# Kernel tuning notes

Measured on AMD Instinct MI355X. Metric: run time of the kernel, lower is better.

## Reference

```python
import jax, jax.numpy as jnp
import numpy as np

M, N, IN_DIM, NITER = 32, 32, 1024, 100
ALPHA, SIGMA = 0.3, 16.0  # sigma default = max(m, n) / 2
BATCH = 16384


def setup_inputs() -> dict:
    key = jax.random.key(0)
    k1, k2 = jax.random.split(key)
    x = jax.random.normal(k1, (BATCH, IN_DIM), dtype=jnp.float32)
    weights = jax.random.normal(k2, (IN_DIM, M * N), dtype=jnp.float32)
    ii, jj = jnp.meshgrid(jnp.arange(M), jnp.arange(N), indexing='ij')
    locations = jnp.stack([ii.ravel(), jj.ravel()], axis=1).astype(jnp.int32)  # (m*n, 2), row-major like the generator
    return {"x": x, "weights": weights, "locations": locations, "current_iter": 10}


def reference(x, weights, locations, current_iter):
    # x: (B, in_dim); weights: (in_dim, m*n); locations: (m*n, 2)
    B = x.shape[0]
    # Euclidean distances from each sample to each neuron, via ||a-b||^2 expansion
    x2 = jnp.sum(x * x, axis=1, keepdims=True)            # (B, 1)
    w2 = jnp.sum(weights * weights, axis=0)[None, :]      # (1, m*n)
    d2 = jnp.clip(x2 + w2 - 2.0 * (x @ weights), 0.0, None)
    dists = jnp.sqrt(d2)                                  # (B, m*n)
    loss_per = jnp.min(dists, axis=1)                     # (B,)
    bmu_index = jnp.argmin(dists, axis=1)                 # (B,)
    iter_correction = 1.0 - current_iter / NITER
    lr = ALPHA * iter_correction
    sigma = SIGMA * iter_correction
    loc_f = locations.astype(jnp.float32)                 # (m*n, 2)
    bmu_loc = loc_f[bmu_index]                            # (B, 2)
    # squared grid distance of every neuron to each sample's BMU
    dsq = jnp.sum((loc_f[None, :, :] - bmu_loc[:, None, :]) ** 2, axis=2)  # (B, m*n)
    lr_locations = jnp.exp(-dsq / (sigma * sigma)) * lr   # (B, m*n)
    # delta[i,k] = (1/B) * sum_b lr_locations[b,k] * (x[b,i] - weights[i,k])
    # computed without materializing the (B, in_dim, m*n) broadcast tensor
    pos = jnp.einsum('bk,bi->ik', lr_locations, x)        # (in_dim, m*n)
    neg = weights * jnp.sum(lr_locations, axis=0)[None, :]
    delta = (pos - neg) / B
    new_weights = weights + delta
    loss = jnp.sum(loss_per) / B
    return loss, new_weights
```

## Files before the change

kernel.cpp:

```cpp
#include <hip/hip_runtime.h>

typedef unsigned short u16;
typedef short bf16x8 __attribute__((ext_vector_type(8)));
typedef float f32x4 __attribute__((ext_vector_type(4)));

#define BATCH   16384
#define INDIM   1024
#define KNEUR   1024

__device__ __forceinline__ u16 f2bf(float f) {
  union { float f; unsigned u; } v; v.f = f;
  unsigned r = v.u + 0x7FFFu + ((v.u >> 16) & 1u);
  return (u16)(r >> 16);
}
__device__ __forceinline__ float bf2f(u16 h) {
  union { unsigned u; float f; } v; v.u = ((unsigned)h) << 16; return v.f;
}

#define GLDS(gp, lp) __builtin_amdgcn_global_load_lds( \
  (const __attribute__((address_space(1))) void*)(gp), \
  (__attribute__((address_space(3))) void*)(lp), 16, 0, 0)

__global__ __launch_bounds__(256)
void k_prep(const float* __restrict__ x, u16* __restrict__ xb, float* __restrict__ x2,
            const float* __restrict__ w, u16* __restrict__ wt, float* __restrict__ w2,
            const int* __restrict__ loc, const int* __restrict__ itp,
            u16* __restrict__ Tb, float* __restrict__ Tf,
            float* __restrict__ Xf, int* __restrict__ cntcur, float* __restrict__ S) {
  __shared__ float tile[64][65];
  __shared__ float red[4][64];
  int bid = blockIdx.x;
  int t = threadIdx.x;
  if (bid < 4096) {
    int row = bid * 4 + (t >> 6);
    int l = t & 63;
    const float* xr = x + (size_t)row * INDIM;
    u16* xbr = xb + (size_t)row * INDIM;
    float s = 0.f;
    #pragma unroll
    for (int seg = 0; seg < 4; ++seg) {
      float4 v = *(const float4*)(xr + seg * 256 + l * 4);
      ushort4 o; o.x = f2bf(v.x); o.y = f2bf(v.y); o.z = f2bf(v.z); o.w = f2bf(v.w);
      *(ushort4*)(xbr + seg * 256 + l * 4) = o;
      s += v.x * v.x + v.y * v.y + v.z * v.z + v.w * v.w;
    }
    for (int m = 32; m; m >>= 1) s += __shfl_xor(s, m, 64);
    if (l == 0) x2[row] = s;
  } else if (bid < 8192) {
    int id = (bid - 4096) * 256 + t;
    int c = id >> 10, k = id & 1023;
    float corr = 1.f - (float)itp[0] / 100.f;
    float lr = 0.3f * corr;
    float sig = 16.f * corr;
    float inv_s2 = 1.f / (sig * sig);
    int di = loc[2 * c] - loc[2 * k];
    int dj = loc[2 * c + 1] - loc[2 * k + 1];
    float v = lr * __expf(-(float)(di * di + dj * dj) * inv_s2);
    Tf[id] = v;
    Tb[id] = f2bf(v);
    Xf[id] = 0.f;
    if (id < 2048) cntcur[id] = 0;
    if (id < 1024) S[id] = 0.f;
  } else if (bid < 8448) {
    int bb = bid - 8192;
    int bi = bb & 15;
    int bj = bb >> 4;
    int tx = t & 63, ty = t >> 6;
    int i0 = bj * 64, k0 = bi * 64;
    for (int r = ty; r < 64; r += 4)
      tile[r][tx] = w[(size_t)(i0 + r) * KNEUR + k0 + tx];
    __syncthreads();
    for (int r = ty; r < 64; r += 4)
      wt[(size_t)(k0 + r) * INDIM + i0 + tx] = f2bf(tile[tx][r]);
  } else {
    int tx = t & 63, ty = t >> 6;
    int k = (bid - 8448) * 64 + tx;
    float s = 0.f;
    for (int i = ty * 256; i < ty * 256 + 256; ++i) {
      float v = w[(size_t)i * KNEUR + k];
      s += v * v;
    }
    red[ty][tx] = s;
    __syncthreads();
    if (ty == 0) w2[k] = red[0][tx] + red[1][tx] + red[2][tx] + red[3][tx];
  }
}

template <int EPI>
__global__ __launch_bounds__(256, 4)
void k_gemm(const u16* __restrict__ A, const u16* __restrict__ Bm,
            const float* __restrict__ x2, const float* __restrict__ w2,
            float* __restrict__ pmin, int* __restrict__ pidx,
            float* __restrict__ P4) {
  __shared__ __align__(16) u16 ldsA[128 * 64];
  __shared__ __align__(16) u16 ldsB[128 * 64];
  __shared__ float s_rv[2][128];
  __shared__ int   s_ri[2][128];

  int bid = blockIdx.x;
  int mb, nb, ktlo, kthi, ks;
  if (EPI == 1) {
    int swz = (bid & 7) * 128 + (bid >> 3);
    mb = swz >> 3; nb = swz & 7;
    ktlo = 0; kthi = 16; ks = 0;
  } else {
    ks = bid & 3;
    int tile = bid >> 2;
    mb = tile >> 3; nb = tile & 7;
    ktlo = ks * 4; kthi = ktlo + 4;
  }
  int lane = threadIdx.x & 63;
  int wid = threadIdx.x >> 6;
  int wr = wid >> 1, wc = wid & 1;

  f32x4 acc[4][4];
  #pragma unroll
  for (int i = 0; i < 4; ++i)
    #pragma unroll
    for (int j = 0; j < 4; ++j) { acc[i][j][0] = 0.f; acc[i][j][1] = 0.f; acc[i][j][2] = 0.f; acc[i][j][3] = 0.f; }

  const size_t rowA0 = (size_t)mb * 128;
  const size_t rowB0 = (size_t)nb * 128;

  for (int kt = ktlo; kt < kthi; ++kt) {
    int k0 = kt * 64;
    __syncthreads();
    #pragma unroll
    for (int q = 0; q < 4; ++q) {
      int p = q * 256 + wid * 64 + lane;
      int row = p >> 3;
      int clog = (p & 7) ^ (row & 7);
      GLDS(A + (rowA0 + row) * 1024 + k0 + clog * 8,
           ldsA + (size_t)(q * 256 + wid * 64) * 8);
    }
    #pragma unroll
    for (int q = 0; q < 4; ++q) {
      int p = q * 256 + wid * 64 + lane;
      int row = p >> 3;
      int clog = (p & 7) ^ (row & 7);
      GLDS(Bm + (rowB0 + row) * 1024 + k0 + clog * 8,
           ldsB + (size_t)(q * 256 + wid * 64) * 8);
    }
    __syncthreads();
    #pragma unroll
    for (int kk = 0; kk < 2; ++kk) {
      bf16x8 af[4], bfr[4];
      #pragma unroll
      for (int mt = 0; mt < 4; ++mt) {
        int row = wr * 64 + mt * 16 + (lane & 15);
        int ch = (kk * 4 + (lane >> 4)) ^ (row & 7);
        af[mt] = *(const bf16x8*)(ldsA + row * 64 + ch * 8);
      }
      #pragma unroll
      for (int nt = 0; nt < 4; ++nt) {
        int row = wc * 64 + nt * 16 + (lane & 15);
        int ch = (kk * 4 + (lane >> 4)) ^ (row & 7);
        bfr[nt] = *(const bf16x8*)(ldsB + row * 64 + ch * 8);
      }
      #pragma unroll
      for (int mt = 0; mt < 4; ++mt)
        #pragma unroll
        for (int nt = 0; nt < 4; ++nt)
          acc[mt][nt] = __builtin_amdgcn_mfma_f32_16x16x32_bf16(af[mt], bfr[nt], acc[mt][nt], 0, 0, 0);
    }
  }

  if (EPI == 1) {
    int g = lane >> 4;
    int li = lane & 15;
    #pragma unroll
    for (int mt = 0; mt < 4; ++mt) {
      #pragma unroll
      for (int r = 0; r < 4; ++r) {
        int rowl = wr * 64 + mt * 16 + g * 4 + r;
        float xv = x2[rowA0 + rowl];
        float v = 1e30f; int vi = 0;
        #pragma unroll
        for (int nt = 0; nt < 4; ++nt) {
          int col = (int)rowB0 + wc * 64 + nt * 16 + li;
          float d2 = xv + w2[col] - 2.f * acc[mt][nt][r];
          if (d2 < v) { v = d2; vi = col; }
        }
        #pragma unroll
        for (int m = 1; m < 16; m <<= 1) {
          float ov = __shfl_xor(v, m, 64);
          int oi = __shfl_xor(vi, m, 64);
          if (ov < v || (ov == v && oi < vi)) { v = ov; vi = oi; }
        }
        if (li == 0) { s_rv[wc][rowl] = v; s_ri[wc][rowl] = vi; }
      }
    }
    __syncthreads();
    int t = threadIdx.x;
    if (t < 128) {
      float v0 = s_rv[0][t], v1 = s_rv[1][t];
      int i0 = s_ri[0][t], i1 = s_ri[1][t];
      float v = v0; int vi = i0;
      if (v1 < v0) { v = v1; vi = i1; }
      size_t brow = rowA0 + t;
      pmin[brow * 8 + nb] = v;
      pidx[brow * 8 + nb] = vi;
    }
  } else {
    float* base = P4 + ((size_t)ks << 20);
    #pragma unroll
    for (int mt = 0; mt < 4; ++mt)
      #pragma unroll
      for (int nt = 0; nt < 4; ++nt)
        #pragma unroll
        for (int r = 0; r < 4; ++r) {
          int i = (int)rowA0 + wr * 64 + mt * 16 + (lane >> 4) * 4 + r;
          int k = (int)rowB0 + wc * 64 + nt * 16 + (lane & 15);
          base[(size_t)i * KNEUR + k] = acc[mt][nt][r];
        }
  }
}

__global__ void k_bmu_count(const float* __restrict__ pmin, const int* __restrict__ pidx,
                            int* __restrict__ bmu, float* __restrict__ lpart,
                            int* __restrict__ cnt) {
  int b = blockIdx.x * 256 + threadIdx.x;
  float v = 1e30f; int vi = 0;
  #pragma unroll
  for (int j = 0; j < 8; ++j) {
    float pv = pmin[(size_t)b * 8 + j];
    if (pv < v) { v = pv; vi = pidx[(size_t)b * 8 + j]; }
  }
  bmu[b] = vi;
  atomicAdd(&cnt[vi], 1);
  float d = sqrtf(fmaxf(v, 0.f));
  __shared__ float red[256];
  red[threadIdx.x] = d;
  __syncthreads();
  for (int s = 128; s > 0; s >>= 1) {
    if (threadIdx.x < s) red[threadIdx.x] += red[threadIdx.x + s];
    __syncthreads();
  }
  if (threadIdx.x == 0) lpart[blockIdx.x] = red[0];
}

__global__ void k_offsets_loss(const int* __restrict__ cnt, int* __restrict__ cursor,
                               float* __restrict__ cntf,
                               const float* __restrict__ lpart, float* __restrict__ out) {
  __shared__ int sc[256];
  int t = threadIdx.x;
  int4 c4 = *(const int4*)(cnt + 4 * t);
  int tsum = c4.x + c4.y + c4.z + c4.w;
  sc[t] = tsum;
  __syncthreads();
  for (int off = 1; off < 256; off <<= 1) {
    int val = sc[t];
    int add = (t >= off) ? sc[t - off] : 0;
    __syncthreads();
    sc[t] = val + add;
    __syncthreads();
  }
  int excl = sc[t] - tsum;
  cursor[4 * t + 0] = excl;
  cursor[4 * t + 1] = excl + c4.x;
  cursor[4 * t + 2] = excl + c4.x + c4.y;
  cursor[4 * t + 3] = excl + c4.x + c4.y + c4.z;
  cntf[4 * t + 0] = (float)c4.x;
  cntf[4 * t + 1] = (float)c4.y;
  cntf[4 * t + 2] = (float)c4.z;
  cntf[4 * t + 3] = (float)c4.w;
  if (t < 64) {
    float l = lpart[t];
    for (int m = 32; m; m >>= 1) l += __shfl_xor(l, m, 64);
    if (t == 0) out[0] = l * (1.f / (float)BATCH);
  }
}

__global__ void k_place_S(const int* __restrict__ bmu, int* __restrict__ cursor,
                          int* __restrict__ perm,
                          const float* __restrict__ cntf, const float* __restrict__ Tf,
                          float* __restrict__ S) {
  int bid = blockIdx.x;
  int t = threadIdx.x;
  if (bid < 64) {
    int b = bid * 256 + t;
    int c = bmu[b];
    int p = atomicAdd(&cursor[c], 1);
    perm[p] = b;
  } else {
    int chunk = bid - 64;
    int cchunk = chunk >> 2;
    int kb = chunk & 3;
    int k = kb * 256 + t;
    float s = 0.f;
    for (int c = cchunk * 64; c < cchunk * 64 + 64; ++c)
      s += cntf[c] * Tf[(size_t)c * KNEUR + k];
    atomicAdd(&S[k], s);
  }
}

__global__ __launch_bounds__(256)
void k_xsum2(const int* __restrict__ perm, const int* __restrict__ bmu,
             const u16* __restrict__ xb, float* __restrict__ Xf) {
  int t = threadIdx.x;
  int m0 = blockIdx.x * 16;
  int pm[16], cl[16];
  #pragma unroll
  for (int j = 0; j < 16; ++j) pm[j] = perm[m0 + j];
  #pragma unroll
  for (int j = 0; j < 16; ++j) cl[j] = bmu[pm[j]];
  float a0 = 0.f, a1 = 0.f, a2 = 0.f, a3 = 0.f;
  int ccur = cl[0];
  #pragma unroll
  for (int j = 0; j < 16; ++j) {
    if (cl[j] != ccur) {
      float* p = Xf + (size_t)ccur * INDIM + 4 * t;
      atomicAdd(p + 0, a0); atomicAdd(p + 1, a1);
      atomicAdd(p + 2, a2); atomicAdd(p + 3, a3);
      a0 = a1 = a2 = a3 = 0.f;
      ccur = cl[j];
    }
    ushort4 v = *(const ushort4*)(xb + (size_t)pm[j] * INDIM + t * 4);
    a0 += bf2f(v.x); a1 += bf2f(v.y); a2 += bf2f(v.z); a3 += bf2f(v.w);
  }
  float* p = Xf + (size_t)ccur * INDIM + 4 * t;
  atomicAdd(p + 0, a0); atomicAdd(p + 1, a1);
  atomicAdd(p + 2, a2); atomicAdd(p + 3, a3);
}

__global__ void k_trans_base(const float* __restrict__ Xf, u16* __restrict__ xst,
                             const float* __restrict__ w, const float* __restrict__ S,
                             float* __restrict__ outw) {
  int bid = blockIdx.x;
  int t = threadIdx.x;
  if (bid < 256) {
    __shared__ float tile[64][65];
    int bc = bid & 15;
    int bi = bid >> 4;
    int tx = t & 63, ty = t >> 6;
    int c0 = bc * 64, i0 = bi * 64;
    for (int r = ty; r < 64; r += 4)
      tile[r][tx] = Xf[(size_t)(c0 + r) * INDIM + i0 + tx];
    __syncthreads();
    for (int r = ty; r < 64; r += 4)
      xst[(size_t)(i0 + r) * KNEUR + c0 + tx] = f2bf(tile[tx][r]);
  } else {
    const float invB = 1.f / (float)BATCH;
    size_t base = ((size_t)(bid - 256) * 256 + t) * 16;
    int k = (int)(base & 1023);
    #pragma unroll
    for (int seg = 0; seg < 4; ++seg) {
      float4 wv = *(const float4*)(w + base + seg * 4);
      float4 sv = *(const float4*)(S + k + seg * 4);
      outw[base + seg * 4 + 0] = wv.x - wv.x * sv.x * invB;
      outw[base + seg * 4 + 1] = wv.y - wv.y * sv.y * invB;
      outw[base + seg * 4 + 2] = wv.z - wv.z * sv.z * invB;
      outw[base + seg * 4 + 3] = wv.w - wv.w * sv.w * invB;
    }
  }
}

__global__ void k_wupd(const float* __restrict__ P4, float* __restrict__ outw) {
  const float invB = 1.f / (float)BATCH;
  int id4 = blockIdx.x * 256 + threadIdx.x;
  size_t base = (size_t)id4 * 4;
  float4 p0 = *(const float4*)(P4 + base);
  float4 p1 = *(const float4*)(P4 + (1u << 20) + base);
  float4 p2 = *(const float4*)(P4 + (2u << 20) + base);
  float4 p3 = *(const float4*)(P4 + (3u << 20) + base);
  outw[base + 0] += (p0.x + p1.x + p2.x + p3.x) * invB;
  outw[base + 1] += (p0.y + p1.y + p2.y + p3.y) * invB;
  outw[base + 2] += (p0.z + p1.z + p2.z + p3.z) * invB;
  outw[base + 3] += (p0.w + p1.w + p2.w + p3.w) * invB;
}

extern "C" void kernel_launch(void* const* d_in, const int* in_sizes, int n_in,
                              void* d_out, int out_size, void* d_ws, size_t ws_size,
                              hipStream_t stream) {
  const float* x = (const float*)d_in[0];
  const float* w = (const float*)d_in[1];
  const int* loc = (const int*)d_in[2];
  const int* it = (const int*)d_in[3];
  float* out = (float*)d_out;

  char* ws = (char*)d_ws;
  size_t off = 0;
  auto alloc = [&](size_t bytes) -> void* {
    void* p = ws + off;
    off += (bytes + 255) & ~(size_t)255;
    return p;
  };
  u16* xb    = (u16*)  alloc((size_t)BATCH * INDIM * 2);
  u16* wt    = (u16*)  alloc((size_t)KNEUR * INDIM * 2);
  u16* Tb    = (u16*)  alloc((size_t)KNEUR * KNEUR * 2);
  float* Tf  = (float*)alloc((size_t)KNEUR * KNEUR * 4);
  u16* xst   = (u16*)  alloc((size_t)INDIM * KNEUR * 2);
  float* x2  = (float*)alloc((size_t)BATCH * 4);
  float* w2  = (float*)alloc((size_t)KNEUR * 4);
  float* pmin= (float*)alloc((size_t)BATCH * 8 * 4);
  int* pidx  = (int*)  alloc((size_t)BATCH * 8 * 4);
  int* bmu   = (int*)  alloc((size_t)BATCH * 4);
  float* cntf= (float*)alloc((size_t)KNEUR * 4);
  float* S   = (float*)alloc((size_t)KNEUR * 4);
  float* lpart=(float*)alloc(64 * 4);
  float* Xf  = (float*)alloc((size_t)KNEUR * INDIM * 4);
  int* cntcur= (int*)  alloc((size_t)2 * KNEUR * 4);
  int* perm  = (int*)  alloc((size_t)BATCH * 4);
  if (off > ws_size) return;

  int* cnt = cntcur;
  int* cursor = cntcur + KNEUR;
  float* outw = out + 1;
  float* P4 = (float*)xb;

  k_prep<<<8464, 256, 0, stream>>>(x, xb, x2, w, wt, w2, loc, it, Tb, Tf, Xf, cntcur, S);
  k_gemm<1><<<1024, 256, 0, stream>>>(xb, wt, x2, w2, pmin, pidx, nullptr);
  k_bmu_count<<<64, 256, 0, stream>>>(pmin, pidx, bmu, lpart, cnt);
  k_offsets_loss<<<1, 256, 0, stream>>>(cnt, cursor, cntf, lpart, out);
  k_place_S<<<128, 256, 0, stream>>>(bmu, cursor, perm, cntf, Tf, S);
  k_xsum2<<<BATCH / 16, 256, 0, stream>>>(perm, bmu, xb, Xf);
  k_trans_base<<<512, 256, 0, stream>>>(Xf, xst, w, S, outw);
  k_gemm<2><<<256, 256, 0, stream>>>(xst, Tb, nullptr, nullptr, nullptr, nullptr, P4);
  k_wupd<<<1024, 256, 0, stream>>>(P4, outw);
}
```

Measured before the change: 148.5 us.

## Replace distance GEMM with 256x256-tile, 8-wave, double-buffered pipelined kernel

Rewrites the main x·W distance GEMM as a 512-thread kernel computing 256x256 output tiles. It double-buffers LDS stages loaded with global_load_lds and runs four quarter-tile phases with explicit barriers, vmcnt waits and setprio around the MFMA bursts. The larger tile halves per-row partial argmin outputs from 8 to 4, so the downstream BMU reduction is updated to match. The aim is to overlap global loads with MFMA work and raise data reuse, at the cost of 128KB LDS per block and a lower block count (256 blocks).

```diff
diff --git a/kernel.cpp b/kernel.cpp
--- a/kernel.cpp
+++ b/kernel.cpp
@@ -20,6 +20,12 @@
 #define GLDS(gp, lp) __builtin_amdgcn_global_load_lds( \
   (const __attribute__((address_space(1))) void*)(gp), \
   (__attribute__((address_space(3))) void*)(lp), 16, 0, 0)
+
+#define RAWBAR() __builtin_amdgcn_s_barrier()
+#define LGKM0() do { asm volatile("s_waitcnt lgkmcnt(0)" ::: "memory"); \
+                     __builtin_amdgcn_sched_barrier(0); } while (0)
+#define VMC6() asm volatile("s_waitcnt vmcnt(6)" ::: "memory")
+#define VMC0() asm volatile("s_waitcnt vmcnt(0)" ::: "memory")
 
 __global__ __launch_bounds__(256)
 void k_prep(const float* __restrict__ x, u16* __restrict__ xb, float* __restrict__ x2,
@@ -86,29 +92,165 @@
   }
 }
 
-template <int EPI>
+__global__ __launch_bounds__(512, 2)
+void k_gemm1_8p(const u16* __restrict__ A, const u16* __restrict__ Bm,
+                const float* __restrict__ x2, const float* __restrict__ w2,
+                float* __restrict__ pmin, int* __restrict__ pidx) {
+  __shared__ __align__(16) u16 lds[2][2][2][128 * 64];
+  __shared__ float s_rv[2][256];
+  __shared__ int   s_ri[2][256];
+
+  int bid = blockIdx.x;
+  int swz = (bid & 7) * 32 + (bid >> 3);
+  int mb = swz >> 2, nb = swz & 3;
+  int tid = threadIdx.x;
+  int lane = tid & 63;
+  int wm = (tid >> 6) >> 1, wn = (tid >> 6) & 1;
+
+  const size_t rowA0 = (size_t)mb * 256;
+  const size_t rowB0 = (size_t)nb * 256;
+
+  auto STAGE = [&](int u, int op, int qh) {
+    if (u >= 16) return;
+    const u16* src = (op == 0) ? (A + (rowA0 + qh * 128) * 1024)
+                               : (Bm + (rowB0 + qh * 128) * 1024);
+    int k0 = u * 64;
+    u16* dst0 = &lds[u & 1][op][qh][0];
+    #pragma unroll
+    for (int j = 0; j < 2; ++j) {
+      int s = j * 512 + tid;
+      int r = s >> 3;
+      int cs = (s & 7) ^ (r & 7);
+      GLDS(src + (size_t)r * 1024 + k0 + cs * 8, dst0 + (size_t)s * 8);
+    }
+  };
+  auto LDA = [&](bf16x8 (&a)[2][2], int db, int qm) {
+    #pragma unroll
+    for (int mt = 0; mt < 2; ++mt)
+      #pragma unroll
+      for (int kk = 0; kk < 2; ++kk) {
+        int row = wm * 32 + mt * 16 + (lane & 15);
+        int ch = (kk * 4 + (lane >> 4)) ^ (row & 7);
+        a[mt][kk] = *(const bf16x8*)(&lds[db][0][qm][row * 64 + ch * 8]);
+      }
+  };
+  auto LDB = [&](bf16x8 (&b)[4][2], int db, int qn) {
+    #pragma unroll
+    for (int nt = 0; nt < 4; ++nt)
+      #pragma unroll
+      for (int kk = 0; kk < 2; ++kk) {
+        int row = wn * 64 + nt * 16 + (lane & 15);
+        int ch = (kk * 4 + (lane >> 4)) ^ (row & 7);
+        b[nt][kk] = *(const bf16x8*)(&lds[db][1][qn][row * 64 + ch * 8]);
+      }
+  };
+
+  f32x4 acc[2][2][2][4];
+  #pragma unroll
+  for (int i = 0; i < 2; ++i)
+    #pragma unroll
+    for (int j = 0; j < 2; ++j)
+      #pragma unroll
+      for (int m = 0; m < 2; ++m)
+        #pragma unroll
+        for (int n = 0; n < 4; ++n) {
+          acc[i][j][m][n][0] = 0.f; acc[i][j][m][n][1] = 0.f;
+          acc[i][j][m][n][2] = 0.f; acc[i][j][m][n][3] = 0.f;
+        }
+
+  bf16x8 a[2][2], b0[4][2], b1[4][2];
+
+  #define PHASE(accq, av, bv) do { \
+    __builtin_amdgcn_s_setprio(1); \
+    _Pragma("unroll") \
+    for (int mt = 0; mt < 2; ++mt) \
+      _Pragma("unroll") \
+      for (int nt = 0; nt < 4; ++nt) \
+        _Pragma("unroll") \
+        for (int kk = 0; kk < 2; ++kk) \
+          accq[mt][nt] = __builtin_amdgcn_mfma_f32_16x16x32_bf16(av[mt][kk], bv[nt][kk], accq[mt][nt], 0, 0, 0); \
+    __builtin_amdgcn_s_setprio(0); \
+  } while (0)
+
+  STAGE(0, 0, 0); STAGE(0, 1, 1); STAGE(0, 0, 1); STAGE(0, 1, 0);
+  STAGE(1, 0, 0); STAGE(1, 1, 1); STAGE(1, 0, 1);
+  VMC6();
+  RAWBAR();
+
+  for (int t = 0; t < 16; ++t) {
+    int db = t & 1;
+    LDA(a, db, 0); LDB(b0, db, 0);
+    STAGE(t + 1, 1, 0);
+    RAWBAR(); LGKM0();
+    PHASE(acc[0][0], a, b0);
+    RAWBAR();
+    LDB(b1, db, 1);
+    STAGE(t + 2, 0, 0);
+    RAWBAR(); LGKM0();
+    PHASE(acc[0][1], a, b1);
+    RAWBAR();
+    LDA(a, db, 1);
+    STAGE(t + 2, 1, 1);
+    RAWBAR(); LGKM0();
+    PHASE(acc[1][1], a, b1);
+    RAWBAR();
+    STAGE(t + 2, 0, 1);
+    RAWBAR(); LGKM0();
+    PHASE(acc[1][0], a, b0);
+    if (t < 14) { VMC6(); } else { VMC0(); }
+    RAWBAR();
+  }
+
+  int g = lane >> 4, li = lane & 15;
+  #pragma unroll
+  for (int qm = 0; qm < 2; ++qm)
+    #pragma unroll
+    for (int mt = 0; mt < 2; ++mt)
+      #pragma unroll
+      for (int rr = 0; rr < 4; ++rr) {
+        int lrow = qm * 128 + wm * 32 + mt * 16 + g * 4 + rr;
+        float xv = x2[rowA0 + lrow];
+        float v = 1e30f; int vi = 0x7fffffff;
+        #pragma unroll
+        for (int qn = 0; qn < 2; ++qn)
+          #pragma unroll
+          for (int nt = 0; nt < 4; ++nt) {
+            int col = (int)rowB0 + qn * 128 + wn * 64 + nt * 16 + li;
+            float d2 = xv + w2[col] - 2.f * acc[qm][qn][mt][nt][rr];
+            if (d2 < v) { v = d2; vi = col; }
+          }
+        #pragma unroll
+        for (int m = 1; m < 16; m <<= 1) {
+          float ov = __shfl_xor(v, m, 64);
+          int oi = __shfl_xor(vi, m, 64);
+          if (ov < v || (ov == v && oi < vi)) { v = ov; vi = oi; }
+        }
+        if (li == 0) { s_rv[wn][lrow] = v; s_ri[wn][lrow] = vi; }
+      }
+  __syncthreads();
+  if (tid < 256) {
+    float v0 = s_rv[0][tid], v1 = s_rv[1][tid];
+    int i0 = s_ri[0][tid], i1 = s_ri[1][tid];
+    float v = v0; int vi = i0;
+    if (v1 < v0 || (v1 == v0 && i1 < i0)) { v = v1; vi = i1; }
+    size_t brow = rowA0 + tid;
+    pmin[brow * 4 + nb] = v;
+    pidx[brow * 4 + nb] = vi;
+  }
+  #undef PHASE
+}
+
 __global__ __launch_bounds__(256, 4)
-void k_gemm(const u16* __restrict__ A, const u16* __restrict__ Bm,
-            const float* __restrict__ x2, const float* __restrict__ w2,
-            float* __restrict__ pmin, int* __restrict__ pidx,
-            float* __restrict__ P4) {
+void k_gemm2(const u16* __restrict__ A, const u16* __restrict__ Bm,
+             float* __restrict__ P4) {
   __shared__ __align__(16) u16 ldsA[128 * 64];
   __shared__ __align__(16) u16 ldsB[128 * 64];
-  __shared__ float s_rv[2][128];
-  __shared__ int   s_ri[2][128];
 
   int bid = blockIdx.x;
-  int mb, nb, ktlo, kthi, ks;
-  if (EPI == 1) {
-    int swz = (bid & 7) * 128 + (bid >> 3);
-    mb = swz >> 3; nb = swz & 7;
-    ktlo = 0; kthi = 16; ks = 0;
-  } else {
-    ks = bid & 3;
-    int tile = bid >> 2;
-    mb = tile >> 3; nb = tile & 7;
-    ktlo = ks * 4; kthi = ktlo + 4;
-  }
+  int ks = bid & 3;
+  int tile = bid >> 2;
+  int mb = tile >> 3, nb = tile & 7;
+  int ktlo = ks * 4, kthi = ktlo + 4;
   int lane = threadIdx.x & 63;
   int wid = threadIdx.x >> 6;
   int wr = wid >> 1, wc = wid & 1;
@@ -165,55 +307,17 @@
     }
   }
 
-  if (EPI == 1) {
-    int g = lane >> 4;
-    int li = lane & 15;
-    #pragma unroll
-    for (int mt = 0; mt < 4; ++mt) {
+  float* base = P4 + ((size_t)ks << 20);
+  #pragma unroll
+  for (int mt = 0; mt < 4; ++mt)
+    #pragma unroll
+    for (int nt = 0; nt < 4; ++nt)
       #pragma unroll
       for (int r = 0; r < 4; ++r) {
-        int rowl = wr * 64 + mt * 16 + g * 4 + r;
-        float xv = x2[rowA0 + rowl];
-        float v = 1e30f; int vi = 0;
-        #pragma unroll
-        for (int nt = 0; nt < 4; ++nt) {
-          int col = (int)rowB0 + wc * 64 + nt * 16 + li;
-          float d2 = xv + w2[col] - 2.f * acc[mt][nt][r];
-          if (d2 < v) { v = d2; vi = col; }
-        }
-        #pragma unroll
-        for (int m = 1; m < 16; m <<= 1) {
-          float ov = __shfl_xor(v, m, 64);
-          int oi = __shfl_xor(vi, m, 64);
-          if (ov < v || (ov == v && oi < vi)) { v = ov; vi = oi; }
-        }
-        if (li == 0) { s_rv[wc][rowl] = v; s_ri[wc][rowl] = vi; }
+        int i = (int)rowA0 + wr * 64 + mt * 16 + (lane >> 4) * 4 + r;
+        int k = (int)rowB0 + wc * 64 + nt * 16 + (lane & 15);
+        base[(size_t)i * KNEUR + k] = acc[mt][nt][r];
       }
-    }
-    __syncthreads();
-    int t = threadIdx.x;
-    if (t < 128) {
-      float v0 = s_rv[0][t], v1 = s_rv[1][t];
-      int i0 = s_ri[0][t], i1 = s_ri[1][t];
-      float v = v0; int vi = i0;
-      if (v1 < v0) { v = v1; vi = i1; }
-      size_t brow = rowA0 + t;
-      pmin[brow * 8 + nb] = v;
-      pidx[brow * 8 + nb] = vi;
-    }
-  } else {
-    float* base = P4 + ((size_t)ks << 20);
-    #pragma unroll
-    for (int mt = 0; mt < 4; ++mt)
-      #pragma unroll
-      for (int nt = 0; nt < 4; ++nt)
-        #pragma unroll
-        for (int r = 0; r < 4; ++r) {
-          int i = (int)rowA0 + wr * 64 + mt * 16 + (lane >> 4) * 4 + r;
-          int k = (int)rowB0 + wc * 64 + nt * 16 + (lane & 15);
-          base[(size_t)i * KNEUR + k] = acc[mt][nt][r];
-        }
-  }
 }
 
 __global__ void k_bmu_count(const float* __restrict__ pmin, const int* __restrict__ pidx,
@@ -222,9 +326,9 @@
   int b = blockIdx.x * 256 + threadIdx.x;
   float v = 1e30f; int vi = 0;
   #pragma unroll
-  for (int j = 0; j < 8; ++j) {
-    float pv = pmin[(size_t)b * 8 + j];
-    if (pv < v) { v = pv; vi = pidx[(size_t)b * 8 + j]; }
+  for (int j = 0; j < 4; ++j) {
+    float pv = pmin[(size_t)b * 4 + j];
+    if (pv < v) { v = pv; vi = pidx[(size_t)b * 4 + j]; }
   }
   bmu[b] = vi;
   atomicAdd(&cnt[vi], 1);
@@ -392,8 +496,8 @@
   u16* xst   = (u16*)  alloc((size_t)INDIM * KNEUR * 2);
   float* x2  = (float*)alloc((size_t)BATCH * 4);
   float* w2  = (float*)alloc((size_t)KNEUR * 4);
-  float* pmin= (float*)alloc((size_t)BATCH * 8 * 4);
-  int* pidx  = (int*)  alloc((size_t)BATCH * 8 * 4);
+  float* pmin= (float*)alloc((size_t)BATCH * 4 * 4);
+  int* pidx  = (int*)  alloc((size_t)BATCH * 4 * 4);
   int* bmu   = (int*)  alloc((size_t)BATCH * 4);
   float* cntf= (float*)alloc((size_t)KNEUR * 4);
   float* S   = (float*)alloc((size_t)KNEUR * 4);
@@ -409,12 +513,12 @@
   float* P4 = (float*)xb;
 
   k_prep<<<8464, 256, 0, stream>>>(x, xb, x2, w, wt, w2, loc, it, Tb, Tf, Xf, cntcur, S);
-  k_gemm<1><<<1024, 256, 0, stream>>>(xb, wt, x2, w2, pmin, pidx, nullptr);
+  k_gemm1_8p<<<256, 512, 0, stream>>>(xb, wt, x2, w2, pmin, pidx);
   k_bmu_count<<<64, 256, 0, stream>>>(pmin, pidx, bmu, lpart, cnt);
   k_offsets_loss<<<1, 256, 0, stream>>>(cnt, cursor, cntf, lpart, out);
   k_place_S<<<128, 256, 0, stream>>>(bmu, cursor, perm, cntf, Tf, S);
   k_xsum2<<<BATCH / 16, 256, 0, stream>>>(perm, bmu, xb, Xf);
   k_trans_base<<<512, 256, 0, stream>>>(Xf, xst, w, S, outw);
-  k_gemm<2><<<256, 256, 0, stream>>>(xst, Tb, nullptr, nullptr, nullptr, nullptr, P4);
+  k_gemm2<<<256, 256, 0, stream>>>(xst, Tb, P4);
   k_wupd<<<1024, 256, 0, stream>>>(P4, outw);
 }
```

After: 142.7 us. -3.9%, faster.
